# Kernel tuning notes

Measured on AMD Instinct MI355X. Metric: run time of the kernel, lower is better.

Reference implementation:

```python
import jax, jax.numpy as jnp
import numpy as np

N_NODES = 50000
N_EDGES = 800000
IN, HID, OUT = 256, 128, 64


def setup_inputs() -> dict:
    key = jax.random.key(0)
    ks = jax.random.split(key, 5)
    return {
        "x": jax.random.normal(ks[0], (N_NODES, IN), dtype=jnp.float32),
        "W1": jax.random.normal(ks[1], (IN, HID), dtype=jnp.float32) / np.sqrt(IN),
        "b1": jnp.zeros((HID,), dtype=jnp.float32),
        "W2": jax.random.normal(ks[2], (HID, OUT), dtype=jnp.float32) / np.sqrt(HID),
        "b2": jnp.zeros((OUT,), dtype=jnp.float32),
        "src": jax.random.randint(ks[3], (N_EDGES,), 0, N_NODES, dtype=jnp.int32),
        "dst": jax.random.randint(ks[4], (N_EDGES,), 0, N_NODES, dtype=jnp.int32),
    }


def _graph_conv(h, W, b, src, dst, norm_src, norm_dst, n_nodes):
    # DGL GraphConv, norm='both': y = D_dst^{-1/2} A D_src^{-1/2} h W + b
    # Project first (smaller feature dim for the SpMM), linearity makes it exact.
    h = h @ W                                     # [N, d_out]
    msg = (h * norm_src[:, None])[src]            # gather per-edge   [E, d_out]
    agg = jax.ops.segment_sum(msg, dst, num_segments=n_nodes)  # [N, d_out]
    return agg * norm_dst[:, None] + b


def reference(x, W1, b1, W2, b2, src, dst):
    n = x.shape[0]
    ones = jnp.ones(src.shape[0], dtype=jnp.float32)
    out_deg = jnp.zeros(n, jnp.float32).at[src].add(ones)
    in_deg = jnp.zeros(n, jnp.float32).at[dst].add(ones)
    norm_src = jax.lax.rsqrt(jnp.maximum(out_deg, 1.0))
    norm_dst = jax.lax.rsqrt(jnp.maximum(in_deg, 1.0))

    h = _graph_conv(x, W1, b1, src, dst, norm_src, norm_dst, n)
    h = jax.nn.relu(h)
    return _graph_conv(h, W2, b2, src, dst, norm_src, norm_dst, n)
```

## Files before the change

### kernel.cpp

```cpp
#include <hip/hip_runtime.h>

#define NN 50000
#define NE 800000
#define NPAD 50176
#define NSLICE 32
#define ESL 25000
#define HPN 25088
#define HPW 12544
#define FPN 12544
#define GB 782
#define NB 196

typedef __attribute__((ext_vector_type(8))) short bf16x8;
typedef __attribute__((ext_vector_type(4))) float f32x4;

__device__ __forceinline__ float u2f(unsigned u) { return __uint_as_float(u); }
__device__ __forceinline__ unsigned f2u(float f) { return __float_as_uint(f); }
__device__ __forceinline__ unsigned short f2bf(float f) {
    unsigned u = f2u(f);
    return (unsigned short)((u + (((u >> 16) & 1u) + 0x7fffu)) >> 16);
}

__global__ __launch_bounds__(256) void wtrans_kernel(
    const float* __restrict__ W1, const float* __restrict__ W2,
    unsigned short* __restrict__ Wh1, unsigned short* __restrict__ Wl1,
    unsigned short* __restrict__ Wh2, unsigned short* __restrict__ Wl2,
    int* __restrict__ done_cnt) {
    if (blockIdx.x == 0 && threadIdx.x == 0) *done_cnt = 0;
    int b = blockIdx.x;
    float w;
    unsigned short *ph, *pl;
    int f;
    if (b < 128) {
        int i = b * 256 + threadIdx.x;
        int k = i >> 7, n = i & 127;
        f = (((n >> 4) * 32 + (k >> 3)) * 16 + (n & 15)) * 8 + (k & 7);
        w = W1[i]; ph = Wh1; pl = Wl1;
    } else {
        int i = (b - 128) * 256 + threadIdx.x;
        int k = i >> 6, n = i & 63;
        f = (((n >> 4) * 16 + (k >> 3)) * 16 + (n & 15)) * 8 + (k & 7);
        w = W2[i]; ph = Wh2; pl = Wl2;
    }
    unsigned u = f2u(w);
    float lo = w - u2f(u & 0xffff0000u);
    ph[f] = (unsigned short)(u >> 16);
    pl[f] = (unsigned short)(f2u(lo) >> 16);
}

__global__ __launch_bounds__(1024) void hist_kernel(
    const int* __restrict__ src, const int* __restrict__ dst,
    unsigned* __restrict__ cnt_sl) {
    __shared__ unsigned lcnt[HPW];
    const int b = blockIdx.x;
    const int side = b & 1;
    const int slice = (b >> 1) & (NSLICE - 1);
    const int part = b >> 6;
    const int* __restrict__ arr = side ? dst : src;
    const int base = part * HPN;
    for (int j = threadIdx.x; j < HPW; j += 1024) lcnt[j] = 0;
    __syncthreads();
    const int e0 = slice * ESL;
    for (int i = e0 + threadIdx.x; i < e0 + ESL; i += 1024) {
        int v = arr[i] - base;
        if ((unsigned)v < (unsigned)HPN)
            atomicAdd(&lcnt[v >> 1], 1u << ((v & 1) * 16));
    }
    __syncthreads();
    unsigned* o = cnt_sl + (size_t)b * HPW;
    for (int j = threadIdx.x; j < HPW; j += 1024) o[j] = lcnt[j];
}

__global__ __launch_bounds__(256) void norm_scanAB_kernel(
    const unsigned* __restrict__ cnt_sl, float* __restrict__ ns,
    float* __restrict__ nd, int* __restrict__ presum,
    int* __restrict__ pref, int* __restrict__ blk_sum,
    int* __restrict__ blk_ofs, int* __restrict__ done_cnt, int n) {
    __shared__ int lds[256];
    __shared__ int is_last;
    int i = blockIdx.x * 256 + threadIdx.x;
    int d_total = 0;
    if (i < n) {
        int part = (i >= HPN) ? 1 : 0;
        int w = (i - part * HPN) >> 1;
        int sh = (i & 1) * 16;
        int s_total = 0;
#pragma unroll
        for (int sl = 0; sl < NSLICE; sl++) {
            int bb = part * 64 + sl * 2;
            s_total += (cnt_sl[(size_t)bb * HPW + w] >> sh) & 0xffff;
            int c = (cnt_sl[(size_t)(bb + 1) * HPW + w] >> sh) & 0xffff;
            presum[sl * NPAD + i] = d_total;
            d_total += c;
        }
        ns[i] = rsqrtf(fmaxf((float)s_total, 1.0f));
        nd[i] = rsqrtf(fmaxf((float)d_total, 1.0f));
    }
    lds[threadIdx.x] = d_total;
    __syncthreads();
    for (int ofs = 1; ofs < 256; ofs <<= 1) {
        int t = (threadIdx.x >= ofs) ? lds[threadIdx.x - ofs] : 0;
        __syncthreads();
        lds[threadIdx.x] += t;
        __syncthreads();
    }
    if (i < n) pref[i] = lds[threadIdx.x] - d_total;
    if (threadIdx.x == 255) blk_sum[blockIdx.x] = lds[255];
    __threadfence();
    if (threadIdx.x == 0) {
        int c = atomicAdd(done_cnt, 1);
        is_last = (c == gridDim.x - 1);
    }
    __syncthreads();
    if (!is_last) return;
    __threadfence();
    int v = (threadIdx.x < gridDim.x) ? blk_sum[threadIdx.x] : 0;
    __syncthreads();
    lds[threadIdx.x] = v;
    __syncthreads();
    for (int ofs = 1; ofs < 256; ofs <<= 1) {
        int t = (threadIdx.x >= ofs) ? lds[threadIdx.x - ofs] : 0;
        __syncthreads();
        lds[threadIdx.x] += t;
        __syncthreads();
    }
    if (threadIdx.x < gridDim.x) blk_ofs[threadIdx.x] = lds[threadIdx.x] - v;
}

__global__ __launch_bounds__(1024) void fill_kernel(
    const int* __restrict__ src, const int* __restrict__ dst,
    const int* __restrict__ pref, const int* __restrict__ blk_ofs,
    const int* __restrict__ presum, int* __restrict__ eidx) {
    __shared__ int cur[FPN];
    const int slice = blockIdx.x >> 2;
    const int part = blockIdx.x & 3;
    const int base = part * FPN;
    for (int j = threadIdx.x; j < FPN; j += 1024) {
        int gi = base + j;
        cur[j] = (gi < NN) ? pref[gi] + blk_ofs[gi >> 8] + presum[slice * NPAD + gi] : 0;
    }
    __syncthreads();
    const int e0 = slice * ESL;
    for (int i = e0 + threadIdx.x; i < e0 + ESL; i += 1024) {
        int v = dst[i] - base;
        if ((unsigned)v < (unsigned)FPN) {
            int pos = atomicAdd(&cur[v], 1);
            eidx[pos] = src[i];
        }
    }
}

__global__ __launch_bounds__(256) void gemm1_kernel(
    const float* __restrict__ A, const unsigned short* __restrict__ Wh,
    const unsigned short* __restrict__ Wl, unsigned short* __restrict__ out, int M) {
    constexpr int N = 128, K = 256;
    constexpr int NT = N / 16, KC = K / 32;
    const int wave = threadIdx.x >> 6;
    const int lane = threadIdx.x & 63;
    const int ln = lane & 15;
    const int qk = lane >> 4;
    const int m0 = blockIdx.x * 64 + wave * 16;
    const int mA = m0 + ln;
    const float* Arow = A + (size_t)(mA < M ? mA : (M - 1)) * K + qk * 8;
    const bf16x8* BH = (const bf16x8*)Wh;
    const bf16x8* BL = (const bf16x8*)Wl;

    f32x4 acc[NT];
#pragma unroll
    for (int t = 0; t < NT; t++) acc[t] = (f32x4){0.f, 0.f, 0.f, 0.f};

#pragma unroll 2
    for (int c = 0; c < KC; ++c) {
        float4 a0 = *(const float4*)(Arow + c * 32);
        float4 a1 = *(const float4*)(Arow + c * 32 + 4);
        float av[8] = {a0.x, a0.y, a0.z, a0.w, a1.x, a1.y, a1.z, a1.w};
        bf16x8 ah, al;
#pragma unroll
        for (int j = 0; j < 8; ++j) {
            unsigned u = f2u(av[j]);
            float lo = av[j] - u2f(u & 0xffff0000u);
            ah[j] = (short)(u >> 16);
            al[j] = (short)(f2u(lo) >> 16);
        }
        const int fb = c * 4 + qk;
#pragma unroll
        for (int t = 0; t < NT; ++t) {
            bf16x8 bh = BH[(t * (K / 8) + fb) * 16 + ln];
            bf16x8 bl = BL[(t * (K / 8) + fb) * 16 + ln];
            acc[t] = __builtin_amdgcn_mfma_f32_16x16x32_bf16(ah, bh, acc[t], 0, 0, 0);
            acc[t] = __builtin_amdgcn_mfma_f32_16x16x32_bf16(ah, bl, acc[t], 0, 0, 0);
            acc[t] = __builtin_amdgcn_mfma_f32_16x16x32_bf16(al, bh, acc[t], 0, 0, 0);
        }
    }
#pragma unroll
    for (int t = 0; t < NT; ++t)
#pragma unroll
        for (int r = 0; r < 4; ++r) {
            int row = m0 + qk * 4 + r;
            if (row < M) out[(size_t)row * N + t * 16 + ln] = f2bf(acc[t][r]);
        }
}

__global__ __launch_bounds__(256) void layer2_kernel(
    const unsigned* __restrict__ hs1, const int* __restrict__ eidx,
    const int* __restrict__ pref, const int* __restrict__ blk_ofs,
    const float* __restrict__ norm_src, const float* __restrict__ norm_dst,
    const float* __restrict__ bias, const unsigned short* __restrict__ Wh,
    const unsigned short* __restrict__ Wl, unsigned short* __restrict__ hs2, int n) {
    __shared__ unsigned lh1[16 * 68];
    const int wave = threadIdx.x >> 6;
    const int lane = threadIdx.x & 63;
    const int nb = blockIdx.x * 16;

    for (int j = 0; j < 4; ++j) {
        const int node = nb + wave * 4 + j;
        float rx = 0.f, ry = 0.f;
        if (node < n) {
            int beg = pref[node] + blk_ofs[node >> 8];
            int end = (node + 1 < n) ? pref[node + 1] + blk_ofs[(node + 1) >> 8] : NE;
            float ax = 0.f, ay = 0.f;
            int e = beg;
            for (; e + 3 < end; e += 4) {
                int s0 = eidx[e], s1 = eidx[e + 1], s2 = eidx[e + 2], s3 = eidx[e + 3];
                float n0 = norm_src[s0], n1 = norm_src[s1];
                float n2 = norm_src[s2], n3 = norm_src[s3];
                unsigned u0 = hs1[(size_t)s0 * 64 + lane];
                unsigned u1 = hs1[(size_t)s1 * 64 + lane];
                unsigned u2 = hs1[(size_t)s2 * 64 + lane];
                unsigned u3 = hs1[(size_t)s3 * 64 + lane];
                ax += n0 * u2f(u0 << 16) + n1 * u2f(u1 << 16) +
                      n2 * u2f(u2 << 16) + n3 * u2f(u3 << 16);
                ay += n0 * u2f(u0 & 0xffff0000u) + n1 * u2f(u1 & 0xffff0000u) +
                      n2 * u2f(u2 & 0xffff0000u) + n3 * u2f(u3 & 0xffff0000u);
            }
            for (; e < end; ++e) {
                int s0 = eidx[e];
                float n0 = norm_src[s0];
                unsigned u0 = hs1[(size_t)s0 * 64 + lane];
                ax += n0 * u2f(u0 << 16);
                ay += n0 * u2f(u0 & 0xffff0000u);
            }
            float sc = norm_dst[node];
            float2 b = ((const float2*)bias)[lane];
            rx = fmaxf(ax * sc + b.x, 0.f);
            ry = fmaxf(ay * sc + b.y, 0.f);
        }
        lh1[(wave * 4 + j) * 68 + lane] = (unsigned)f2bf(rx) | ((unsigned)f2bf(ry) << 16);
    }
    __syncthreads();

    const int ln = lane & 15;
    const int qk = lane >> 4;
    const int t = wave;
    const bf16x8* BH = (const bf16x8*)Wh;
    const bf16x8* BL = (const bf16x8*)Wl;
    f32x4 acc = (f32x4){0.f, 0.f, 0.f, 0.f};
#pragma unroll
    for (int c = 0; c < 4; ++c) {
        bf16x8 ah = *(const bf16x8*)&lh1[ln * 68 + c * 16 + qk * 4];
        const int fb = c * 4 + qk;
        bf16x8 bh = BH[(t * 16 + fb) * 16 + ln];
        bf16x8 bl = BL[(t * 16 + fb) * 16 + ln];
        acc = __builtin_amdgcn_mfma_f32_16x16x32_bf16(ah, bh, acc, 0, 0, 0);
        acc = __builtin_amdgcn_mfma_f32_16x16x32_bf16(ah, bl, acc, 0, 0, 0);
    }
#pragma unroll
    for (int r = 0; r < 4; ++r) {
        int node = nb + qk * 4 + r;
        if (node < n) hs2[(size_t)node * 64 + t * 16 + ln] = f2bf(acc[r]);
    }
}

__global__ __launch_bounds__(256) void gather64_kernel(
    const unsigned* __restrict__ hs, const int* __restrict__ eidx,
    const int* __restrict__ pref, const int* __restrict__ blk_ofs,
    const float* __restrict__ norm_src, const float* __restrict__ norm_dst,
    const float* __restrict__ bias, float* __restrict__ out, int n) {
    int wave = (blockIdx.x * blockDim.x + threadIdx.x) >> 6;
    int lane = threadIdx.x & 63;
    if (wave >= n) return;
    int beg = pref[wave] + blk_ofs[wave >> 8];
    int end = (wave + 1 < n) ? pref[wave + 1] + blk_ofs[(wave + 1) >> 8] : NE;
    int half = lane >> 5;
    int dim = lane & 31;
    float ax = 0.f, ay = 0.f;
    int e = beg + half;
    for (; e + 2 < end; e += 4) {
        int s0 = eidx[e], s1 = eidx[e + 2];
        float n0 = norm_src[s0], n1 = norm_src[s1];
        unsigned u0 = hs[(size_t)s0 * 32 + dim];
        unsigned u1 = hs[(size_t)s1 * 32 + dim];
        ax += n0 * u2f(u0 << 16) + n1 * u2f(u1 << 16);
        ay += n0 * u2f(u0 & 0xffff0000u) + n1 * u2f(u1 & 0xffff0000u);
    }
    if (e < end) {
        int s0 = eidx[e];
        float n0 = norm_src[s0];
        unsigned u0 = hs[(size_t)s0 * 32 + dim];
        ax += n0 * u2f(u0 << 16);
        ay += n0 * u2f(u0 & 0xffff0000u);
    }
    ax += __shfl_xor(ax, 32);
    ay += __shfl_xor(ay, 32);
    if (half == 0) {
        float sc = norm_dst[wave];
        float2 b = ((const float2*)bias)[dim];
        ((float2*)out)[(size_t)wave * 32 + dim] =
            make_float2(ax * sc + b.x, ay * sc + b.y);
    }
}

extern "C" void kernel_launch(void* const* d_in, const int* in_sizes, int n_in,
                              void* d_out, int out_size, void* d_ws, size_t ws_size,
                              hipStream_t stream) {
    const float* x  = (const float*)d_in[0];
    const float* W1 = (const float*)d_in[1];
    const float* b1 = (const float*)d_in[2];
    const float* W2 = (const float*)d_in[3];
    const float* b2 = (const float*)d_in[4];
    const int* src  = (const int*)d_in[5];
    const int* dst  = (const int*)d_in[6];
    float* out = (float*)d_out;
    char* ws = (char*)d_ws;

    float* norm_src = (float*)(ws);
    float* norm_dst = (float*)(ws + 4 * 50176);
    int*   pref     = (int*)(ws + 4 * 100352);
    int*   blk_sum  = (int*)(ws + 4 * 150528);
    int*   blk_ofs  = (int*)(ws + 4 * 150784);
    int*   done_cnt = (int*)(ws + 4 * 151040);
    int*   eidx     = (int*)(ws + 4 * 151296);
    unsigned short* Wh1 = (unsigned short*)(ws + 4 * 951296);
    unsigned short* Wl1 = (unsigned short*)(ws + 4 * 967680);
    unsigned short* Wh2 = (unsigned short*)(ws + 4 * 984064);
    unsigned short* Wl2 = (unsigned short*)(ws + 4 * 988160);
    unsigned short* hs1 = (unsigned short*)(ws + 4 * 992256);
    unsigned short* hs2 = (unsigned short*)(ws + 4 * 4192256);
    unsigned* cnt_sl    = (unsigned*)(ws + 4 * 5792256);
    int* presum         = (int*)(ws + 4 * 7397888);

    wtrans_kernel<<<160, 256, 0, stream>>>(W1, W2, Wh1, Wl1, Wh2, Wl2, done_cnt);

    hist_kernel<<<128, 1024, 0, stream>>>(src, dst, cnt_sl);
    gemm1_kernel<<<GB, 256, 0, stream>>>(x, Wh1, Wl1, hs1, NN);

    norm_scanAB_kernel<<<NB, 256, 0, stream>>>(cnt_sl, norm_src, norm_dst,
                                               presum, pref, blk_sum, blk_ofs,
                                               done_cnt, NN);
    fill_kernel<<<128, 1024, 0, stream>>>(src, dst, pref, blk_ofs, presum, eidx);

    layer2_kernel<<<3125, 256, 0, stream>>>(
        (const unsigned*)hs1, eidx, pref, blk_ofs, norm_src, norm_dst, b1,
        Wh2, Wl2, hs2, NN);

    gather64_kernel<<<12500, 256, 0, stream>>>(
        (const unsigned*)hs2, eidx, pref, blk_ofs, norm_src, norm_dst, b2, out, NN);
}
```

Before: 250.9 us.

## Fold source-degree normalization into GEMM epilogues and merge weight prep with histogram

Multiplies norm_src into the projected rows when they are written (in gemm1 and layer2), so the per-edge gathers no longer load norm_src at a random index for every edge. The gather loops are unrolled further (8 edges in layer2, 4 per half-wave in gather64) to keep more loads in flight. The weight-split kernel is merged into the histogram kernel to save a launch, and gemm1 is moved after the norm scan so it can read norm_src, which serializes it behind the scan. Rounding the pre-scaled values to bf16 changes numerics slightly.

```diff
diff --git a/kernel.cpp b/kernel.cpp
--- a/kernel.cpp
+++ b/kernel.cpp
@@ -21,38 +21,37 @@
     return (unsigned short)((u + (((u >> 16) & 1u) + 0x7fffu)) >> 16);
 }
 
-__global__ __launch_bounds__(256) void wtrans_kernel(
+__global__ __launch_bounds__(1024) void hist_wtrans_kernel(
+    const int* __restrict__ src, const int* __restrict__ dst,
+    unsigned* __restrict__ cnt_sl,
     const float* __restrict__ W1, const float* __restrict__ W2,
     unsigned short* __restrict__ Wh1, unsigned short* __restrict__ Wl1,
     unsigned short* __restrict__ Wh2, unsigned short* __restrict__ Wl2,
     int* __restrict__ done_cnt) {
     if (blockIdx.x == 0 && threadIdx.x == 0) *done_cnt = 0;
-    int b = blockIdx.x;
-    float w;
-    unsigned short *ph, *pl;
-    int f;
-    if (b < 128) {
-        int i = b * 256 + threadIdx.x;
-        int k = i >> 7, n = i & 127;
-        f = (((n >> 4) * 32 + (k >> 3)) * 16 + (n & 15)) * 8 + (k & 7);
-        w = W1[i]; ph = Wh1; pl = Wl1;
-    } else {
-        int i = (b - 128) * 256 + threadIdx.x;
-        int k = i >> 6, n = i & 63;
-        f = (((n >> 4) * 16 + (k >> 3)) * 16 + (n & 15)) * 8 + (k & 7);
-        w = W2[i]; ph = Wh2; pl = Wl2;
-    }
-    unsigned u = f2u(w);
-    float lo = w - u2f(u & 0xffff0000u);
-    ph[f] = (unsigned short)(u >> 16);
-    pl[f] = (unsigned short)(f2u(lo) >> 16);
-}
-
-__global__ __launch_bounds__(1024) void hist_kernel(
-    const int* __restrict__ src, const int* __restrict__ dst,
-    unsigned* __restrict__ cnt_sl) {
+    const int b = blockIdx.x;
+    if (b >= 128) {
+        float w;
+        unsigned short *ph, *pl;
+        int f;
+        if (b < 160) {
+            int i = (b - 128) * 1024 + threadIdx.x;
+            int k = i >> 7, n = i & 127;
+            f = (((n >> 4) * 32 + (k >> 3)) * 16 + (n & 15)) * 8 + (k & 7);
+            w = W1[i]; ph = Wh1; pl = Wl1;
+        } else {
+            int i = (b - 160) * 1024 + threadIdx.x;
+            int k = i >> 6, n = i & 63;
+            f = (((n >> 4) * 16 + (k >> 3)) * 16 + (n & 15)) * 8 + (k & 7);
+            w = W2[i]; ph = Wh2; pl = Wl2;
+        }
+        unsigned u = f2u(w);
+        float lo = w - u2f(u & 0xffff0000u);
+        ph[f] = (unsigned short)(u >> 16);
+        pl[f] = (unsigned short)(f2u(lo) >> 16);
+        return;
+    }
     __shared__ unsigned lcnt[HPW];
-    const int b = blockIdx.x;
     const int side = b & 1;
     const int slice = (b >> 1) & (NSLICE - 1);
     const int part = b >> 6;
@@ -152,7 +151,8 @@
 
 __global__ __launch_bounds__(256) void gemm1_kernel(
     const float* __restrict__ A, const unsigned short* __restrict__ Wh,
-    const unsigned short* __restrict__ Wl, unsigned short* __restrict__ out, int M) {
+    const unsigned short* __restrict__ Wl, const float* __restrict__ norm_src,
+    unsigned short* __restrict__ out, int M) {
     constexpr int N = 128, K = 256;
     constexpr int NT = N / 16, KC = K / 32;
     const int wave = threadIdx.x >> 6;
@@ -192,12 +192,18 @@
             acc[t] = __builtin_amdgcn_mfma_f32_16x16x32_bf16(al, bh, acc[t], 0, 0, 0);
         }
     }
+    float sc[4];
+#pragma unroll
+    for (int r = 0; r < 4; ++r) {
+        int row = m0 + qk * 4 + r;
+        sc[r] = (row < M) ? norm_src[row] : 0.f;
+    }
 #pragma unroll
     for (int t = 0; t < NT; ++t)
 #pragma unroll
         for (int r = 0; r < 4; ++r) {
             int row = m0 + qk * 4 + r;
-            if (row < M) out[(size_t)row * N + t * 16 + ln] = f2bf(acc[t][r]);
+            if (row < M) out[(size_t)row * N + t * 16 + ln] = f2bf(acc[t][r] * sc[r]);
         }
 }
 
@@ -220,25 +226,35 @@
             int end = (node + 1 < n) ? pref[node + 1] + blk_ofs[(node + 1) >> 8] : NE;
             float ax = 0.f, ay = 0.f;
             int e = beg;
+            for (; e + 7 < end; e += 8) {
+                unsigned u0 = hs1[(size_t)eidx[e] * 64 + lane];
+                unsigned u1 = hs1[(size_t)eidx[e + 1] * 64 + lane];
+                unsigned u2 = hs1[(size_t)eidx[e + 2] * 64 + lane];
+                unsigned u3 = hs1[(size_t)eidx[e + 3] * 64 + lane];
+                unsigned u4 = hs1[(size_t)eidx[e + 4] * 64 + lane];
+                unsigned u5 = hs1[(size_t)eidx[e + 5] * 64 + lane];
+                unsigned u6 = hs1[(size_t)eidx[e + 6] * 64 + lane];
+                unsigned u7 = hs1[(size_t)eidx[e + 7] * 64 + lane];
+                ax += u2f(u0 << 16) + u2f(u1 << 16) + u2f(u2 << 16) + u2f(u3 << 16) +
+                      u2f(u4 << 16) + u2f(u5 << 16) + u2f(u6 << 16) + u2f(u7 << 16);
+                ay += u2f(u0 & 0xffff0000u) + u2f(u1 & 0xffff0000u) +
+                      u2f(u2 & 0xffff0000u) + u2f(u3 & 0xffff0000u) +
+                      u2f(u4 & 0xffff0000u) + u2f(u5 & 0xffff0000u) +
+                      u2f(u6 & 0xffff0000u) + u2f(u7 & 0xffff0000u);
+            }
             for (; e + 3 < end; e += 4) {
-                int s0 = eidx[e], s1 = eidx[e + 1], s2 = eidx[e + 2], s3 = eidx[e + 3];
-                float n0 = norm_src[s0], n1 = norm_src[s1];
-                float n2 = norm_src[s2], n3 = norm_src[s3];
-                unsigned u0 = hs1[(size_t)s0 * 64 + lane];
-                unsigned u1 = hs1[(size_t)s1 * 64 + lane];
-                unsigned u2 = hs1[(size_t)s2 * 64 + lane];
-                unsigned u3 = hs1[(size_t)s3 * 64 + lane];
-                ax += n0 * u2f(u0 << 16) + n1 * u2f(u1 << 16) +
-                      n2 * u2f(u2 << 16) + n3 * u2f(u3 << 16);
-                ay += n0 * u2f(u0 & 0xffff0000u) + n1 * u2f(u1 & 0xffff0000u) +
-                      n2 * u2f(u2 & 0xffff0000u) + n3 * u2f(u3 & 0xffff0000u);
+                unsigned u0 = hs1[(size_t)eidx[e] * 64 + lane];
+                unsigned u1 = hs1[(size_t)eidx[e + 1] * 64 + lane];
+                unsigned u2 = hs1[(size_t)eidx[e + 2] * 64 + lane];
+                unsigned u3 = hs1[(size_t)eidx[e + 3] * 64 + lane];
+                ax += u2f(u0 << 16) + u2f(u1 << 16) + u2f(u2 << 16) + u2f(u3 << 16);
+                ay += u2f(u0 & 0xffff0000u) + u2f(u1 & 0xffff0000u) +
+                      u2f(u2 & 0xffff0000u) + u2f(u3 & 0xffff0000u);
             }
             for (; e < end; ++e) {
-                int s0 = eidx[e];
-                float n0 = norm_src[s0];
-                unsigned u0 = hs1[(size_t)s0 * 64 + lane];
-                ax += n0 * u2f(u0 << 16);
-                ay += n0 * u2f(u0 & 0xffff0000u);
+                unsigned u0 = hs1[(size_t)eidx[e] * 64 + lane];
+                ax += u2f(u0 << 16);
+                ay += u2f(u0 & 0xffff0000u);
             }
             float sc = norm_dst[node];
             float2 b = ((const float2*)bias)[lane];
@@ -267,15 +283,16 @@
 #pragma unroll
     for (int r = 0; r < 4; ++r) {
         int node = nb + qk * 4 + r;
-        if (node < n) hs2[(size_t)node * 64 + t * 16 + ln] = f2bf(acc[r]);
+        if (node < n)
+            hs2[(size_t)node * 64 + t * 16 + ln] = f2bf(acc[r] * norm_src[node]);
     }
 }
 
 __global__ __launch_bounds__(256) void gather64_kernel(
     const unsigned* __restrict__ hs, const int* __restrict__ eidx,
     const int* __restrict__ pref, const int* __restrict__ blk_ofs,
-    const float* __restrict__ norm_src, const float* __restrict__ norm_dst,
-    const float* __restrict__ bias, float* __restrict__ out, int n) {
+    const float* __restrict__ norm_dst, const float* __restrict__ bias,
+    float* __restrict__ out, int n) {
     int wave = (blockIdx.x * blockDim.x + threadIdx.x) >> 6;
     int lane = threadIdx.x & 63;
     if (wave >= n) return;
@@ -285,20 +302,19 @@
     int dim = lane & 31;
     float ax = 0.f, ay = 0.f;
     int e = beg + half;
-    for (; e + 2 < end; e += 4) {
-        int s0 = eidx[e], s1 = eidx[e + 2];
-        float n0 = norm_src[s0], n1 = norm_src[s1];
-        unsigned u0 = hs[(size_t)s0 * 32 + dim];
-        unsigned u1 = hs[(size_t)s1 * 32 + dim];
-        ax += n0 * u2f(u0 << 16) + n1 * u2f(u1 << 16);
-        ay += n0 * u2f(u0 & 0xffff0000u) + n1 * u2f(u1 & 0xffff0000u);
-    }
-    if (e < end) {
-        int s0 = eidx[e];
-        float n0 = norm_src[s0];
-        unsigned u0 = hs[(size_t)s0 * 32 + dim];
-        ax += n0 * u2f(u0 << 16);
-        ay += n0 * u2f(u0 & 0xffff0000u);
+    for (; e + 6 < end; e += 8) {
+        unsigned u0 = hs[(size_t)eidx[e] * 32 + dim];
+        unsigned u1 = hs[(size_t)eidx[e + 2] * 32 + dim];
+        unsigned u2 = hs[(size_t)eidx[e + 4] * 32 + dim];
+        unsigned u3 = hs[(size_t)eidx[e + 6] * 32 + dim];
+        ax += u2f(u0 << 16) + u2f(u1 << 16) + u2f(u2 << 16) + u2f(u3 << 16);
+        ay += u2f(u0 & 0xffff0000u) + u2f(u1 & 0xffff0000u) +
+              u2f(u2 & 0xffff0000u) + u2f(u3 & 0xffff0000u);
+    }
+    for (; e < end; e += 2) {
+        unsigned u0 = hs[(size_t)eidx[e] * 32 + dim];
+        ax += u2f(u0 << 16);
+        ay += u2f(u0 & 0xffff0000u);
     }
     ax += __shfl_xor(ax, 32);
     ay += __shfl_xor(ay, 32);
@@ -339,14 +355,15 @@
     unsigned* cnt_sl    = (unsigned*)(ws + 4 * 5792256);
     int* presum         = (int*)(ws + 4 * 7397888);
 
-    wtrans_kernel<<<160, 256, 0, stream>>>(W1, W2, Wh1, Wl1, Wh2, Wl2, done_cnt);
-
-    hist_kernel<<<128, 1024, 0, stream>>>(src, dst, cnt_sl);
-    gemm1_kernel<<<GB, 256, 0, stream>>>(x, Wh1, Wl1, hs1, NN);
+    hist_wtrans_kernel<<<168, 1024, 0, stream>>>(src, dst, cnt_sl, W1, W2,
+                                                 Wh1, Wl1, Wh2, Wl2, done_cnt);
 
     norm_scanAB_kernel<<<NB, 256, 0, stream>>>(cnt_sl, norm_src, norm_dst,
                                                presum, pref, blk_sum, blk_ofs,
                                                done_cnt, NN);
+
+    gemm1_kernel<<<GB, 256, 0, stream>>>(x, Wh1, Wl1, norm_src, hs1, NN);
+
     fill_kernel<<<128, 1024, 0, stream>>>(src, dst, pref, blk_ofs, presum, eidx);
 
     layer2_kernel<<<3125, 256, 0, stream>>>(
@@ -354,5 +371,5 @@
         Wh2, Wl2, hs2, NN);
 
     gather64_kernel<<<12500, 256, 0, stream>>>(
-        (const unsigned*)hs2, eidx, pref, blk_ofs, norm_src, norm_dst, b2, out, NN);
-}
+        (const unsigned*)hs2, eidx, pref, blk_ofs, norm_dst, b2, out, NN);
+}
```

Result: faster. 238.6 us (-4.9%).
